# Kernel tuning notes

Hardware: AMD Instinct MI355X
Metric: run time of the kernel (lower is better)

The kernel has to match this reference:

```python
import jax, jax.numpy as jnp
import numpy as np
import math

K = 3            # max_rings
N_COMP = K + 2   # rings + center + background
RING_S = 0.02
BG_SIGMA = 0.94
CENTER_SIGMA = 0.01
NOISE_CAP = 0.15
COND_DIM, H_DIM = 64, 128
D_IN = COND_DIM + H_DIM


def setup_inputs() -> dict:
    key = jax.random.key(0)
    ks = jax.random.split(key, 12)
    sc = lambda fan_in: 1.0 / np.sqrt(fan_in)
    return {
        "c": jax.random.normal(ks[0], (1, COND_DIM), jnp.float32),
        "h": jax.random.normal(ks[1], (1, H_DIM), jnp.float32),
        # logits MLP: [D_IN, 128, 128, N_COMP]
        "W1": jax.random.normal(ks[2], (D_IN, 128), jnp.float32) * sc(D_IN),
        "b1": jnp.zeros((128,), jnp.float32),
        "W2": jax.random.normal(ks[3], (128, 128), jnp.float32) * sc(128),
        "b2": jnp.zeros((128,), jnp.float32),
        "W3": jax.random.normal(ks[4], (128, N_COMP), jnp.float32) * sc(128),
        "b3": jnp.zeros((N_COMP,), jnp.float32),
        # center_radius head: mus [K,2], Rs [K]
        "W_mu": jax.random.normal(ks[5], (D_IN, K * 2), jnp.float32) * sc(D_IN),
        "b_mu": jnp.zeros((K * 2,), jnp.float32),
        "W_R": jax.random.normal(ks[6], (D_IN, K), jnp.float32) * sc(D_IN),
        "b_R": jnp.ones((K,), jnp.float32) * 0.5,
        "N": 8388608,
    }


def _capped_weights(x, W1, b1, W2, b2, W3, b3):
    z = jax.nn.silu(x @ W1 + b1)
    z = jax.nn.silu(z @ W2 + b2)
    w = jax.nn.softmax(z @ W3 + b3, axis=-1)          # [1, N_COMP]
    w_bg = jnp.minimum(w[..., -1:], NOISE_CAP)
    w_rest = w[..., :-1]
    rest_sum = jnp.maximum(w_rest.sum(-1, keepdims=True), 1e-8)
    w_rest = w_rest * (1.0 - w_bg) / rest_sum
    return jnp.concatenate([w_rest, w_bg], axis=-1) + 1e-8


def reference(c, h, W1, b1, W2, b2, W3, b3, W_mu, b_mu, W_R, b_R, N):
    x = jnp.concatenate([c, h], axis=-1)              # [1, D_IN]
    w = _capped_weights(x, W1, b1, W2, b2, W3, b3)[0]  # [N_COMP]
    mus = (x @ W_mu + b_mu).reshape(K, 2)             # [K, 2]
    Rs = (x @ W_R + b_R)[0]                           # [K]

    key = jax.random.key(42)
    k_cat, k_th, k_r, k_eps = jax.random.split(key, 4)
    idx = jax.random.categorical(k_cat, jnp.log(w), shape=(N,))   # [N]
    jr = jnp.minimum(idx, K - 1)                      # safe ring index

    theta = jax.random.uniform(k_th, (N,), jnp.float32) * (2.0 * math.pi)
    r = Rs[jr] + RING_S * jax.random.normal(k_r, (N,), jnp.float32)
    ring_xy = jnp.stack([r * jnp.cos(theta), r * jnp.sin(theta)], axis=-1) + mus[jr]

    eps = jax.random.normal(k_eps, (N, 2), jnp.float32)
    center_xy = mus[0] + CENTER_SIGMA * eps
    bg_xy = mus[0] + BG_SIGMA * eps

    is_ring = (idx < K)[:, None]
    is_center = (idx == K)[:, None]
    xy = jnp.where(is_ring, ring_xy, jnp.where(is_center, center_xy, bg_xy))
    return xy, idx
```

## Files before the change

kernel.cpp:

```cpp
#include <hip/hip_runtime.h>
#include <math.h>

#define TFROT(v, r) (((v) << (r)) | ((v) >> (32 - (r))))

__device__ __forceinline__ void tf_block(unsigned k0, unsigned k1,
                                         unsigned x0, unsigned x1,
                                         unsigned &o0, unsigned &o1) {
  unsigned ks2 = k0 ^ k1 ^ 0x1BD11BDAu;
  x0 += k0; x1 += k1;
  x0 += x1; x1 = TFROT(x1, 13); x1 ^= x0;
  x0 += x1; x1 = TFROT(x1, 15); x1 ^= x0;
  x0 += x1; x1 = TFROT(x1, 26); x1 ^= x0;
  x0 += x1; x1 = TFROT(x1,  6); x1 ^= x0;
  x0 += k1; x1 += ks2 + 1u;
  x0 += x1; x1 = TFROT(x1, 17); x1 ^= x0;
  x0 += x1; x1 = TFROT(x1, 29); x1 ^= x0;
  x0 += x1; x1 = TFROT(x1, 16); x1 ^= x0;
  x0 += x1; x1 = TFROT(x1, 24); x1 ^= x0;
  x0 += ks2; x1 += k0 + 2u;
  x0 += x1; x1 = TFROT(x1, 13); x1 ^= x0;
  x0 += x1; x1 = TFROT(x1, 15); x1 ^= x0;
  x0 += x1; x1 = TFROT(x1, 26); x1 ^= x0;
  x0 += x1; x1 = TFROT(x1,  6); x1 ^= x0;
  x0 += k0; x1 += k1 + 3u;
  x0 += x1; x1 = TFROT(x1, 17); x1 ^= x0;
  x0 += x1; x1 = TFROT(x1, 29); x1 ^= x0;
  x0 += x1; x1 = TFROT(x1, 16); x1 ^= x0;
  x0 += x1; x1 = TFROT(x1, 24); x1 ^= x0;
  x0 += k1; x1 += ks2 + 4u;
  x0 += x1; x1 = TFROT(x1, 13); x1 ^= x0;
  x0 += x1; x1 = TFROT(x1, 15); x1 ^= x0;
  x0 += x1; x1 = TFROT(x1, 26); x1 ^= x0;
  x0 += x1; x1 = TFROT(x1,  6); x1 ^= x0;
  x0 += ks2; x1 += k0 + 5u;
  o0 = x0; o1 = x1;
}

__device__ __forceinline__ unsigned tf_bits32(unsigned k0, unsigned k1, unsigned i) {
  unsigned o0, o1;
  tf_block(k0, k1, 0u, i, o0, o1);
  return o0 ^ o1;
}

__device__ __forceinline__ float xla_exp_f32(float x) {
#pragma clang fp contract(off)
  const float kHi = 88.3762626647950f;
  const float kLo = -88.3762626647949f;
  const float kLog2e = 1.44269504088896341f;
  const float kC1 = 0.693359375f;
  const float kC2 = -2.12194440e-4f;
  const float p0 = 1.9875691500e-4f, p1 = 1.3981999507e-3f,
              p2 = 8.3334519073e-3f, p3 = 4.1665795894e-2f,
              p4 = 1.6666665459e-1f, p5 = 5.0000001201e-1f;
  float xc = fminf(fmaxf(x, kLo), kHi);
  float t = xc * kLog2e;
  t = t + 0.5f;
  float fx = floorf(t);
  float tmp = kC1 * fx;
  float z = kC2 * fx;
  float xr = xc - tmp;
  xr = xr - z;
  z = xr * xr;
  float y = p0 * xr;  y = y + p1;
  y = y * xr;  y = y + p2;
  y = y * xr;  y = y + p3;
  y = y * xr;  y = y + p4;
  y = y * xr;  y = y + p5;
  y = y * z;   y = y + xr;
  y = 1.0f + y;
  int emm0 = (int)fx;
  emm0 = (emm0 + 0x7f) << 23;
  float two_n = __int_as_float(emm0);
  float res = y * two_n;
  return fmaxf(res, x);
}

__device__ __forceinline__ float xla_log_f32(float x) {
#pragma clang fp contract(off)
  const float kSqrtHf = 0.707106781186547524f;
  const float p0 = 7.0376836292e-2f,  p1 = -1.1514610310e-1f,
              p2 = 1.1676998740e-1f,  p3 = -1.2420140846e-1f,
              p4 = 1.4249322787e-1f,  p5 = -1.6668057665e-1f,
              p6 = 2.0000714765e-1f,  p7 = -2.4999993993e-1f,
              p8 = 3.3333331174e-1f;
  const float q1 = -2.12194440e-4f, q2 = 0.693359375f;
  float t0 = fmaxf(x, __uint_as_float(0x00800000u));
  unsigned ib = __float_as_uint(t0);
  int ei = (int)(ib >> 23) - 0x7f;
  float e = (float)ei;
  e = e + 1.0f;
  t0 = __uint_as_float((ib & 0x807fffffu) | 0x3f000000u);
  bool m = (t0 < kSqrtHf);
  float tmp1 = m ? t0 : 0.0f;
  t0 = t0 - 1.0f;
  e = e - (m ? 1.0f : 0.0f);
  t0 = t0 + tmp1;
  float x2 = t0 * t0;
  float x3 = x2 * t0;
  float y, y1, y2;
  y  = p0 * t0;  y  = y  + p1;
  y1 = p3 * t0;  y1 = y1 + p4;
  y2 = p6 * t0;  y2 = y2 + p7;
  y  = y  * t0;  y  = y  + p2;
  y1 = y1 * t0;  y1 = y1 + p5;
  y2 = y2 * t0;  y2 = y2 + p8;
  y  = y * x3;   y  = y + y1;
  y  = y * x3;   y  = y + y2;
  y  = y * x3;
  y1 = e * q1;
  float tmp2 = x2 * 0.5f;
  y = y + y1;
  t0 = t0 - tmp2;
  y2 = e * q2;
  t0 = t0 + y;
  t0 = t0 + y2;
  return t0;
}

__device__ __forceinline__ float bits_to_f01(unsigned b) {
#pragma clang fp contract(off)
  return __uint_as_float((b >> 9) | 0x3f800000u) - 1.0f;
}

__device__ __forceinline__ float erfinv_f(float x) {
  float t = fmaf(-x, x, 1.0f);
  float w = -__logf(t);
  float p;
  if (w < 5.0f) {
    float v = w - 2.5f;
    p = 2.81022636e-08f;
    p = fmaf(p, v, 3.43273939e-07f);
    p = fmaf(p, v, -3.5233877e-06f);
    p = fmaf(p, v, -4.39150654e-06f);
    p = fmaf(p, v, 0.00021858087f);
    p = fmaf(p, v, -0.00125372503f);
    p = fmaf(p, v, -0.00417768164f);
    p = fmaf(p, v, 0.246640727f);
    p = fmaf(p, v, 1.50140941f);
  } else {
    float v = __fsqrt_rn(w) - 3.0f;
    p = -0.000200214257f;
    p = fmaf(p, v, 0.000100950558f);
    p = fmaf(p, v, 0.00134934322f);
    p = fmaf(p, v, -0.00367342844f);
    p = fmaf(p, v, 0.00573950773f);
    p = fmaf(p, v, -0.0076224613f);
    p = fmaf(p, v, 0.00943887047f);
    p = fmaf(p, v, 1.00167406f);
    p = fmaf(p, v, 2.83297682f);
  }
  return p * x;
}

struct Params {
  double mu[6];
  double Rs[3];
  float logits[5];
  float invw[5];
  unsigned keys[8];
};

__global__ void prep_kernel(const float* __restrict__ c, const float* __restrict__ h,
                            const float* __restrict__ W1, const float* __restrict__ b1,
                            const float* __restrict__ W2, const float* __restrict__ b2,
                            const float* __restrict__ W3, const float* __restrict__ b3,
                            const float* __restrict__ Wmu, const float* __restrict__ bmu,
                            const float* __restrict__ WR, const float* __restrict__ bR,
                            Params* __restrict__ P) {
#pragma clang fp contract(off)
  __shared__ float xs[192], z1[128], z2[128], z3[5];
  int t = threadIdx.x;
  if (t < 64) xs[t] = c[t];
  else if (t < 192) xs[t] = h[t - 64];
  __syncthreads();
  if (t < 128) {
    float acc = 0.0f;
    for (int k = 0; k < 192; ++k) { float pr = xs[k] * W1[k * 128 + t]; acc = acc + pr; }
    acc = acc + b1[t];
    float ex = xla_exp_f32(-acc);
    float den = 1.0f + ex;
    float sg = 1.0f / den;
    z1[t] = acc * sg;
  }
  __syncthreads();
  if (t < 128) {
    float acc = 0.0f;
    for (int k = 0; k < 128; ++k) { float pr = z1[k] * W2[k * 128 + t]; acc = acc + pr; }
    acc = acc + b2[t];
    float ex = xla_exp_f32(-acc);
    float den = 1.0f + ex;
    float sg = 1.0f / den;
    z2[t] = acc * sg;
  }
  __syncthreads();
  if (t < 5) {
    float acc = 0.0f;
    for (int k = 0; k < 128; ++k) { float pr = z2[k] * W3[k * 5 + t]; acc = acc + pr; }
    z3[t] = acc + b3[t];
  }
  if (t < 6) {
    double acc = 0.0;
    for (int k = 0; k < 192; ++k) acc += (double)xs[k] * (double)Wmu[k * 6 + t];
    P->mu[t] = acc + (double)bmu[t];
  }
  if (t < 3) {
    double acc = 0.0;
    for (int k = 0; k < 192; ++k) acc += (double)xs[k] * (double)WR[k * 3 + t];
    P->Rs[t] = acc + (double)bR[t];
  }
  __syncthreads();
  if (t == 0) {
    float mx = z3[0];
    for (int j = 1; j < 5; ++j) mx = fmaxf(mx, z3[j]);
    float ev[5];
    float ssum = 0.0f;
    for (int j = 0; j < 5; ++j) {
      float d = z3[j] - mx;
      ev[j] = xla_exp_f32(d);
      ssum = ssum + ev[j];
    }
    float w[5];
    for (int j = 0; j < 5; ++j) w[j] = ev[j] / ssum;
    float wbg = fminf(w[4], 0.15f);
    float rsum = 0.0f;
    for (int j = 0; j < 4; ++j) rsum = rsum + w[j];
    float rs = fmaxf(rsum, 1e-8f);
    float om = 1.0f - wbg;
    float wf[5];
    for (int j = 0; j < 4; ++j) {
      float a = w[j] * om;
      float bq = a / rs;
      wf[j] = bq + 1e-8f;
    }
    wf[4] = wbg + 1e-8f;
    for (int j = 0; j < 5; ++j) {
      P->logits[j] = xla_log_f32(wf[j]);
      P->invw[j] = 1.0f / wf[j];
    }
    unsigned a0, a1;
    tf_block(0u, 42u, 0u, 0u, a0, a1); P->keys[0] = a0; P->keys[1] = a1;
    tf_block(0u, 42u, 0u, 1u, a0, a1); P->keys[2] = a0; P->keys[3] = a1;
    tf_block(0u, 42u, 0u, 2u, a0, a1); P->keys[4] = a0; P->keys[5] = a1;
    tf_block(0u, 42u, 0u, 3u, a0, a1); P->keys[6] = a0; P->keys[7] = a1;
  }
}

__global__ void __launch_bounds__(256)
sample_kernel(const Params* __restrict__ P, float* __restrict__ out, int N) {
#pragma clang fp contract(off)
  const float TINYF = __uint_as_float(0x00800000u);
  const float LOF   = __uint_as_float(0xBF7FFFFFu);
  const float SQRT2F = 1.4142135623730951f;

  float lg[5], cw[5];
  float muf[6], Rsf[3];
  unsigned ky[8];
#pragma unroll
  for (int j = 0; j < 5; ++j) lg[j] = P->logits[j];
#pragma unroll
  for (int j = 0; j < 5; ++j) cw[j] = P->invw[j];
#pragma unroll
  for (int j = 0; j < 6; ++j) muf[j] = (float)P->mu[j];
#pragma unroll
  for (int j = 0; j < 3; ++j) Rsf[j] = (float)P->Rs[j];
#pragma unroll
  for (int j = 0; j < 8; ++j) ky[j] = P->keys[j];

  int T = gridDim.x * blockDim.x;
  for (int s = blockIdx.x * blockDim.x + threadIdx.x; s < N; s += T) {
    unsigned base = 5u * (unsigned)s;
    unsigned bb[5];
    int bi = 0;
    float m1 = __builtin_inff();
    float m2 = __builtin_inff();
#pragma unroll
    for (int j = 0; j < 5; ++j) {
      unsigned b = tf_bits32(ky[0], ky[1], base + (unsigned)j);
      bb[j] = b;
      float u0 = bits_to_f01(b);
      float e2 = -__log2f(u0);
      float m = e2 * cw[j];
      bool lt = m < m1;
      float old1 = m1;
      m1 = lt ? m : m1;
      m2 = lt ? old1 : fminf(m2, m);
      bi = lt ? j : bi;
    }
    bool slow = (m2 - m1 < 1e-3f * m2) || (m1 < 1e-4f) || (m2 > 1e37f);
    if (slow) {
      int best = 0;
      float bestv = -__builtin_inff();
#pragma unroll
      for (int j = 0; j < 5; ++j) {
        float u0 = bits_to_f01(bb[j]);
        float u = u0 + TINYF;
        u = fmaxf(TINYF, u);
        float l1 = xla_log_f32(u);
        float nl1 = -l1;
        float l2 = xla_log_f32(nl1);
        float g = -l2;
        float sc = g + lg[j];
        if (sc > bestv) { bestv = sc; best = j; }
      }
      bi = best;
    }

    bool ring = bi < 3;
    unsigned sU = (unsigned)s;
    unsigned cA = ring ? sU : 2u * sU;
    unsigned cB = ring ? sU : 2u * sU + 1u;
    unsigned kA0 = ring ? ky[2] : ky[6];
    unsigned kA1 = ring ? ky[3] : ky[7];
    unsigned kB0 = ring ? ky[4] : ky[6];
    unsigned kB1 = ring ? ky[5] : ky[7];
    unsigned bA = tf_bits32(kA0, kA1, cA);
    unsigned bB = tf_bits32(kB0, kB1, cB);

    float a01 = bits_to_f01(bA);
    float b01 = bits_to_f01(bB);
    float uB = fmaxf(LOF, fmaf(b01, 2.0f, LOF));
    float nB = SQRT2F * erfinv_f(uB);

    float Rb = (bi == 0) ? Rsf[0] : ((bi == 1) ? Rsf[1] : Rsf[2]);
    float mxr = (bi == 0) ? muf[0] : ((bi == 1) ? muf[2] : muf[4]);
    float myr = (bi == 0) ? muf[1] : ((bi == 1) ? muf[3] : muf[5]);
    float r = fmaf(0.02f, nB, Rb);
    float rx = fmaf(r, __builtin_amdgcn_cosf(a01), mxr);
    float ry = fmaf(r, __builtin_amdgcn_sinf(a01), myr);

    float uA = fmaxf(LOF, fmaf(a01, 2.0f, LOF));
    float nA = SQRT2F * erfinv_f(uA);
    float sg = (bi == 3) ? 0.01f : 0.94f;
    float ex = fmaf(sg, nA, muf[0]);
    float ey = fmaf(sg, nB, muf[1]);

    float ox = ring ? rx : ex;
    float oy = ring ? ry : ey;

    reinterpret_cast<float2*>(out)[s] = make_float2(ox, oy);
    out[(size_t)2 * (size_t)N + (size_t)s] = (float)bi;
  }
}

extern "C" void kernel_launch(void* const* d_in, const int* in_sizes, int n_in,
                              void* d_out, int out_size, void* d_ws, size_t ws_size,
                              hipStream_t stream) {
  const float* c   = (const float*)d_in[0];
  const float* h   = (const float*)d_in[1];
  const float* W1  = (const float*)d_in[2];
  const float* b1  = (const float*)d_in[3];
  const float* W2  = (const float*)d_in[4];
  const float* b2  = (const float*)d_in[5];
  const float* W3  = (const float*)d_in[6];
  const float* b3  = (const float*)d_in[7];
  const float* Wmu = (const float*)d_in[8];
  const float* bmu = (const float*)d_in[9];
  const float* WR  = (const float*)d_in[10];
  const float* bR  = (const float*)d_in[11];
  (void)in_sizes; (void)n_in; (void)ws_size;

  int N = out_size / 3;
  Params* P = (Params*)d_ws;

  hipLaunchKernelGGL(prep_kernel, dim3(1), dim3(256), 0, stream,
                     c, h, W1, b1, W2, b2, W3, b3, Wmu, bmu, WR, bR, P);
  int blocks = 4096;
  hipLaunchKernelGGL(sample_kernel, dim3(blocks), dim3(256), 0, stream,
                     P, (float*)d_out, N);
}
```

Before: 193.8 us.

## Fuse parameter MLP into sampling kernel, recomputing per block

Result: slower. 200.9 us (+3.7%).

```diff
diff --git a/kernel.cpp b/kernel.cpp
--- a/kernel.cpp
+++ b/kernel.cpp
@@ -1,7 +1,7 @@
 #include <hip/hip_runtime.h>
 #include <math.h>
 
-#define TFROT(v, r) (((v) << (r)) | ((v) >> (32 - (r))))
+#define TFROT(v, r) __builtin_amdgcn_alignbit((v), (v), 32 - (r))
 
 __device__ __forceinline__ void tf_block(unsigned k0, unsigned k1,
                                          unsigned x0, unsigned x1,
@@ -152,27 +152,30 @@
   return p * x;
 }
 
-struct Params {
-  double mu[6];
-  double Rs[3];
-  float logits[5];
-  float invw[5];
-  unsigned keys[8];
-};
-
-__global__ void prep_kernel(const float* __restrict__ c, const float* __restrict__ h,
-                            const float* __restrict__ W1, const float* __restrict__ b1,
-                            const float* __restrict__ W2, const float* __restrict__ b2,
-                            const float* __restrict__ W3, const float* __restrict__ b3,
-                            const float* __restrict__ Wmu, const float* __restrict__ bmu,
-                            const float* __restrict__ WR, const float* __restrict__ bR,
-                            Params* __restrict__ P) {
+__global__ void __launch_bounds__(256)
+fused_kernel(const float* __restrict__ c, const float* __restrict__ h,
+             const float* __restrict__ W1, const float* __restrict__ b1,
+             const float* __restrict__ W2, const float* __restrict__ b2,
+             const float* __restrict__ W3, const float* __restrict__ b3,
+             const float* __restrict__ Wmu, const float* __restrict__ bmu,
+             const float* __restrict__ WR, const float* __restrict__ bR,
+             float* __restrict__ out, int N) {
 #pragma clang fp contract(off)
-  __shared__ float xs[192], z1[128], z2[128], z3[5];
-  int t = threadIdx.x;
+  __shared__ float xs[192], z1[128], z2[128], z3[5], s_ev[5];
+  __shared__ float s_lg[5], s_cw[5], s_mu[6], s_Rs[3];
+  __shared__ unsigned s_ky[8];
+  const int t = threadIdx.x;
+
   if (t < 64) xs[t] = c[t];
   else if (t < 192) xs[t] = h[t - 64];
-  __syncthreads();
+  if (t >= 192 && t < 196) {
+    unsigned a0, a1;
+    tf_block(0u, 42u, 0u, (unsigned)(t - 192), a0, a1);
+    s_ky[2 * (t - 192) + 0] = a0;
+    s_ky[2 * (t - 192) + 1] = a1;
+  }
+  __syncthreads();
+
   if (t < 128) {
     float acc = 0.0f;
     for (int k = 0; k < 192; ++k) { float pr = xs[k] * W1[k * 128 + t]; acc = acc + pr; }
@@ -183,6 +186,7 @@
     z1[t] = acc * sg;
   }
   __syncthreads();
+
   if (t < 128) {
     float acc = 0.0f;
     for (int k = 0; k < 128; ++k) { float pr = z1[k] * W2[k * 128 + t]; acc = acc + pr; }
@@ -193,81 +197,87 @@
     z2[t] = acc * sg;
   }
   __syncthreads();
+
   if (t < 5) {
     float acc = 0.0f;
     for (int k = 0; k < 128; ++k) { float pr = z2[k] * W3[k * 5 + t]; acc = acc + pr; }
     z3[t] = acc + b3[t];
   }
   if (t < 6) {
-    double acc = 0.0;
-    for (int k = 0; k < 192; ++k) acc += (double)xs[k] * (double)Wmu[k * 6 + t];
-    P->mu[t] = acc + (double)bmu[t];
+    double a0 = 0.0, a1 = 0.0, a2 = 0.0, a3 = 0.0;
+    for (int k = 0; k < 192; k += 4) {
+      a0 += (double)xs[k + 0] * (double)Wmu[(k + 0) * 6 + t];
+      a1 += (double)xs[k + 1] * (double)Wmu[(k + 1) * 6 + t];
+      a2 += (double)xs[k + 2] * (double)Wmu[(k + 2) * 6 + t];
+      a3 += (double)xs[k + 3] * (double)Wmu[(k + 3) * 6 + t];
+    }
+    s_mu[t] = (float)(((a0 + a1) + (a2 + a3)) + (double)bmu[t]);
   }
   if (t < 3) {
-    double acc = 0.0;
-    for (int k = 0; k < 192; ++k) acc += (double)xs[k] * (double)WR[k * 3 + t];
-    P->Rs[t] = acc + (double)bR[t];
-  }
-  __syncthreads();
-  if (t == 0) {
+    double a0 = 0.0, a1 = 0.0, a2 = 0.0, a3 = 0.0;
+    for (int k = 0; k < 192; k += 4) {
+      a0 += (double)xs[k + 0] * (double)WR[(k + 0) * 3 + t];
+      a1 += (double)xs[k + 1] * (double)WR[(k + 1) * 3 + t];
+      a2 += (double)xs[k + 2] * (double)WR[(k + 2) * 3 + t];
+      a3 += (double)xs[k + 3] * (double)WR[(k + 3) * 3 + t];
+    }
+    s_Rs[t] = (float)(((a0 + a1) + (a2 + a3)) + (double)bR[t]);
+  }
+  __syncthreads();
+
+  if (t < 5) {
     float mx = z3[0];
     for (int j = 1; j < 5; ++j) mx = fmaxf(mx, z3[j]);
-    float ev[5];
-    float ssum = 0.0f;
-    for (int j = 0; j < 5; ++j) {
-      float d = z3[j] - mx;
-      ev[j] = xla_exp_f32(d);
-      ssum = ssum + ev[j];
-    }
-    float w[5];
-    for (int j = 0; j < 5; ++j) w[j] = ev[j] / ssum;
-    float wbg = fminf(w[4], 0.15f);
+    float d = z3[t] - mx;
+    s_ev[t] = xla_exp_f32(d);
+  }
+  __syncthreads();
+  if (t < 5) {
+    float ev0 = s_ev[0], ev1 = s_ev[1], ev2 = s_ev[2], ev3 = s_ev[3], ev4 = s_ev[4];
+    float ssum = ev0 + ev1;
+    ssum = ssum + ev2;
+    ssum = ssum + ev3;
+    ssum = ssum + ev4;
+    float w0 = ev0 / ssum, w1 = ev1 / ssum, w2 = ev2 / ssum,
+          w3 = ev3 / ssum, w4 = ev4 / ssum;
+    float wbg = fminf(w4, 0.15f);
     float rsum = 0.0f;
-    for (int j = 0; j < 4; ++j) rsum = rsum + w[j];
+    rsum = rsum + w0; rsum = rsum + w1; rsum = rsum + w2; rsum = rsum + w3;
     float rs = fmaxf(rsum, 1e-8f);
     float om = 1.0f - wbg;
-    float wf[5];
-    for (int j = 0; j < 4; ++j) {
-      float a = w[j] * om;
+    float wt;
+    if (t < 4) {
+      float wj = (t == 0) ? w0 : ((t == 1) ? w1 : ((t == 2) ? w2 : w3));
+      float a = wj * om;
       float bq = a / rs;
-      wf[j] = bq + 1e-8f;
-    }
-    wf[4] = wbg + 1e-8f;
-    for (int j = 0; j < 5; ++j) {
-      P->logits[j] = xla_log_f32(wf[j]);
-      P->invw[j] = 1.0f / wf[j];
-    }
-    unsigned a0, a1;
-    tf_block(0u, 42u, 0u, 0u, a0, a1); P->keys[0] = a0; P->keys[1] = a1;
-    tf_block(0u, 42u, 0u, 1u, a0, a1); P->keys[2] = a0; P->keys[3] = a1;
-    tf_block(0u, 42u, 0u, 2u, a0, a1); P->keys[4] = a0; P->keys[5] = a1;
-    tf_block(0u, 42u, 0u, 3u, a0, a1); P->keys[6] = a0; P->keys[7] = a1;
-  }
-}
-
-__global__ void __launch_bounds__(256)
-sample_kernel(const Params* __restrict__ P, float* __restrict__ out, int N) {
-#pragma clang fp contract(off)
+      wt = bq + 1e-8f;
+    } else {
+      wt = wbg + 1e-8f;
+    }
+    s_lg[t] = xla_log_f32(wt);
+    s_cw[t] = 1.0f / wt;
+  }
+  __syncthreads();
+
   const float TINYF = __uint_as_float(0x00800000u);
   const float LOF   = __uint_as_float(0xBF7FFFFFu);
   const float SQRT2F = 1.4142135623730951f;
 
-  float lg[5], cw[5];
-  float muf[6], Rsf[3];
+  float lg[5], cw[5], muf[6], Rsf[3];
   unsigned ky[8];
 #pragma unroll
-  for (int j = 0; j < 5; ++j) lg[j] = P->logits[j];
-#pragma unroll
-  for (int j = 0; j < 5; ++j) cw[j] = P->invw[j];
-#pragma unroll
-  for (int j = 0; j < 6; ++j) muf[j] = (float)P->mu[j];
-#pragma unroll
-  for (int j = 0; j < 3; ++j) Rsf[j] = (float)P->Rs[j];
-#pragma unroll
-  for (int j = 0; j < 8; ++j) ky[j] = P->keys[j];
+  for (int j = 0; j < 5; ++j) lg[j] = s_lg[j];
+#pragma unroll
+  for (int j = 0; j < 5; ++j) cw[j] = s_cw[j];
+#pragma unroll
+  for (int j = 0; j < 6; ++j) muf[j] = s_mu[j];
+#pragma unroll
+  for (int j = 0; j < 3; ++j) Rsf[j] = s_Rs[j];
+#pragma unroll
+  for (int j = 0; j < 8; ++j) ky[j] = s_ky[j];
 
   int T = gridDim.x * blockDim.x;
-  for (int s = blockIdx.x * blockDim.x + threadIdx.x; s < N; s += T) {
+  for (int s = blockIdx.x * blockDim.x + t; s < N; s += T) {
     unsigned base = 5u * (unsigned)s;
     unsigned bb[5];
     int bi = 0;
@@ -321,7 +331,7 @@
     float uB = fmaxf(LOF, fmaf(b01, 2.0f, LOF));
     float nB = SQRT2F * erfinv_f(uB);
 
-    float Rb = (bi == 0) ? Rsf[0] : ((bi == 1) ? Rsf[1] : Rsf[2]);
+    float Rb  = (bi == 0) ? Rsf[0] : ((bi == 1) ? Rsf[1] : Rsf[2]);
     float mxr = (bi == 0) ? muf[0] : ((bi == 1) ? muf[2] : muf[4]);
     float myr = (bi == 0) ? muf[1] : ((bi == 1) ? muf[3] : muf[5]);
     float r = fmaf(0.02f, nB, Rb);
@@ -357,14 +367,11 @@
   const float* bmu = (const float*)d_in[9];
   const float* WR  = (const float*)d_in[10];
   const float* bR  = (const float*)d_in[11];
-  (void)in_sizes; (void)n_in; (void)ws_size;
+  (void)in_sizes; (void)n_in; (void)d_ws; (void)ws_size;
 
   int N = out_size / 3;
-  Params* P = (Params*)d_ws;
-
-  hipLaunchKernelGGL(prep_kernel, dim3(1), dim3(256), 0, stream,
-                     c, h, W1, b1, W2, b2, W3, b3, Wmu, bmu, WR, bR, P);
   int blocks = 4096;
-  hipLaunchKernelGGL(sample_kernel, dim3(blocks), dim3(256), 0, stream,
-                     P, (float*)d_out, N);
-}
+  hipLaunchKernelGGL(fused_kernel, dim3(blocks), dim3(256), 0, stream,
+                     c, h, W1, b1, W2, b2, W3, b3, Wmu, bmu, WR, bR,
+                     (float*)d_out, N);
+}
```
